# Optimization experiments

Measured on AMD Instinct MI355X. Metric: run time of the kernel, lower is better.

The kernel has to match this reference:

```python
import jax, jax.numpy as jnp
import numpy as np

B, T, A, P = 128, 128, 16, 4
D, H, Q, QI, V = 256, 512, 128, 512, 64
NUM_TRICKS = 13
SIGNAL_PHASE = 1
# static phase routing: contiguous blocks of T/P positions per phase (phase_mask buffer)
PHASE_ID = (np.arange(T) * P // T).astype(np.int32)
_DECAY = 0.6
_nt_left = NUM_TRICKS - np.arange(NUM_TRICKS, dtype=np.float32)
P_SIGNAL = ((1.0 - _DECAY) / (1.0 - _DECAY ** _nt_left)).astype(np.float32)


def setup_inputs() -> dict:
    key = jax.random.key(0)
    ks = jax.random.split(key, 12)
    a = jax.random.randint(ks[0], (B, T, A, 3), 0, V, dtype=jnp.int32)
    pad = (jax.random.uniform(ks[1], (B, T, A)) < 0.3) & (jnp.arange(A) >= 1)
    valid_actions = jnp.where(pad[..., None], -1, a)
    phase = jnp.broadcast_to(jnp.asarray(PHASE_ID), (B, T)).astype(jnp.int32)
    trick = jax.random.randint(ks[2], (B, T), 0, NUM_TRICKS, dtype=jnp.int32)
    backbone_embed = jax.random.normal(ks[3], (B, T, QI), jnp.float32)
    s = lambda k, shape, fan: jax.random.normal(k, shape, jnp.float32) / np.float32(np.sqrt(fan))
    return dict(
        backbone_embed=backbone_embed, valid_actions=valid_actions, phase=phase, trick=trick,
        emb0=s(ks[4], (V, D), D), emb1=s(ks[5], (V, D), D), emb2=s(ks[6], (V, D), D),
        ln_g=jnp.ones((D,), jnp.float32), ln_b=jnp.zeros((D,), jnp.float32),
        kW1=s(ks[7], (P, D, H), D), kb1=jnp.zeros((P, H), jnp.float32),
        kW2=s(ks[8], (P, H, H), H), kb2=jnp.zeros((P, H), jnp.float32),
        kW3=s(ks[9], (P, H, Q), H), kb3=jnp.zeros((P, Q), jnp.float32),
        qW=s(ks[10], (P, QI, Q), QI), qb=jnp.zeros((P, Q), jnp.float32),
    )


def _forward(backbone_embed, valid_actions, phase, trick,
             emb0, emb1, emb2, ln_g, ln_b,
             kW1, kb1, kW2, kb2, kW3, kb3, qW, qb):
    pid = PHASE_ID  # static (T,) routing -> gather per-position phase params (same math as mask gather/scatter)
    idx = jnp.clip(valid_actions, 0, V - 1)
    x = emb0[idx[..., 0]] + emb1[idx[..., 1]] + emb2[idx[..., 2]]  # (B,T,A,D) action embed
    mu = jnp.mean(x, -1, keepdims=True)
    var = jnp.var(x, -1, keepdims=True)
    x = (x - mu) * jax.lax.rsqrt(var + 1e-5) * ln_g + ln_b  # key LayerNorm
    # phase-branched key MLP (BranchedFF over MLP)
    h = jax.nn.relu(jnp.einsum('btad,tdh->btah', x, kW1[pid]) + kb1[pid][None, :, None, :])
    h = jax.nn.relu(jnp.einsum('btah,thg->btag', h, kW2[pid]) + kb2[pid][None, :, None, :])
    keyv = jnp.einsum('btah,thq->btaq', h, kW3[pid]) + kb3[pid][None, :, None, :]  # (B,T,A,Q)
    # phase-branched query Linear (BranchedFF over Linear)
    query = jnp.einsum('btd,tdq->btq', backbone_embed, qW[pid]) + qb[pid][None]  # (B,T,Q)
    attn = jnp.einsum('btq,btaq->bta', query, keyv) / np.float32(np.sqrt(Q))
    invalid = valid_actions[..., 0] == -1
    attn = jnp.where(invalid, -jnp.inf, attn)
    # no-signal log-weight
    n_valid = jnp.sum(~invalid, -1).astype(attn.dtype)  # (B,T)
    p_s = jnp.asarray(P_SIGNAL)[trick]
    wgt = jnp.log(jnp.maximum((1.0 - p_s) / p_s * (n_valid - 1.0), 1e-5))
    wgt = jnp.where(n_valid == 1.0, 0.0, wgt)
    attn = attn.at[..., 0].add(jnp.where(phase == SIGNAL_PHASE, wgt, 0.0))
    return jax.nn.log_softmax(attn, axis=-1)


def reference(backbone_embed, valid_actions, phase, trick,
              emb0, emb1, emb2, ln_g, ln_b,
              kW1, kb1, kW2, kb2, kW3, kb3, qW, qb):
    return _forward(backbone_embed, valid_actions, phase, trick,
                    emb0, emb1, emb2, ln_g, ln_b,
                    kW1, kb1, kW2, kb2, kW3, kb3, qW, qb)
```

## Files before the change

### kernel.cpp

```cpp
#include <hip/hip_runtime.h>
#include <hip/hip_bf16.h>
#include <cmath>

constexpr int Bc = 128, Tc = 128, Ac = 16;
constexpr int Dc = 256, Hc = 512, Qc = 128, QIc = 512, Vc = 64, NTk = 13;
constexpr float NEG_BIG = -1e30f;
constexpr float ACT_SCALE = 16.f;
constexpr float ACC_SCALE = 1.f / 256.f;
constexpr float ACC_TO_ACT = 1.f / 16.f;

typedef unsigned int uint;
typedef uint uint2v __attribute__((ext_vector_type(2)));
typedef int i32x8 __attribute__((ext_vector_type(8)));
typedef float f32x4 __attribute__((ext_vector_type(4)));
typedef float f32x16 __attribute__((ext_vector_type(16)));

#define MFMA128(a, b, c) __builtin_amdgcn_mfma_scale_f32_16x16x128_f8f6f4( \
    (a), (b), (c), 0, 0, 0, 0x7F7F7F7F, 0, 0x7F7F7F7F)
#define MFMA32(a, b, c) __builtin_amdgcn_mfma_scale_f32_32x32x64_f8f6f4( \
    (a), (b), (c), 0, 0, 0, 0x7F7F7F7F, 0, 0x7F7F7F7F)

__device__ __forceinline__ unsigned short f2bfu(float f) {
  __hip_bfloat16 h = __float2bfloat16(f);
  return *(unsigned short*)&h;
}
__device__ __forceinline__ float bf2f(short s) {
  return __uint_as_float(((unsigned)(unsigned short)s) << 16);
}
__device__ __forceinline__ uint pack4_fp8(float a, float b, float c, float d) {
  uint v = 0;
  v = __builtin_amdgcn_cvt_pk_fp8_f32(a, b, v, 0);
  v = __builtin_amdgcn_cvt_pk_fp8_f32(c, d, v, 1);
  return v;
}

__global__ void transform_all(const float* __restrict__ kW1, const float* __restrict__ kW2,
                              const float* __restrict__ kW3, const float* __restrict__ qW,
                              int* __restrict__ kW1f, int* __restrict__ kW2f,
                              int* __restrict__ kW3f, int* __restrict__ qWf) {
  int id = blockIdx.x * 256 + threadIdx.x;
  int jh = id >> 16;
  int gid = id & 65535;
  const float* W;
  int* dst;
  int NT, KC, N, local;
  bool big;
  if (gid < 16384) {
    W = kW1; dst = kW1f; NT = 16; KC = 4; N = 512; local = gid; big = true;
  } else if (gid < 49152) {
    W = kW2; dst = kW2f; NT = 16; KC = 8; N = 512; local = gid - 16384; big = true;
  } else if (gid < 57344) {
    W = kW3; dst = kW3f; NT = 4; KC = 8; N = 128; local = gid - 49152; big = true;
  } else {
    W = qW; dst = qWf; NT = 8; KC = 4; N = 128; local = gid - 57344; big = false;
  }
  int lane = local & 63;
  int frag = local >> 6;
  int kc = frag % KC;
  int rest = frag / KC;
  int nt = rest % NT;
  int pp = rest / NT;
  int K = KC * (big ? 64 : 128);
  int n, k0;
  if (big) { n = nt * 32 + (lane & 31); k0 = kc * 64 + (lane >> 5) * 32; }
  else     { n = nt * 16 + (lane & 15); k0 = kc * 128 + (lane >> 4) * 32; }
  k0 += jh * 16;
  const float* src = W + ((size_t)pp * K + k0) * N + n;
  int4 v;
  int vv[4];
#pragma unroll
  for (int jj = 0; jj < 4; ++jj) {
    float f0 = src[(size_t)(4 * jj + 0) * N] * ACT_SCALE;
    float f1 = src[(size_t)(4 * jj + 1) * N] * ACT_SCALE;
    float f2 = src[(size_t)(4 * jj + 2) * N] * ACT_SCALE;
    float f3 = src[(size_t)(4 * jj + 3) * N] * ACT_SCALE;
    vv[jj] = (int)pack4_fp8(f0, f1, f2, f3);
  }
  v.x = vv[0]; v.y = vv[1]; v.z = vv[2]; v.w = vv[3];
  *(int4*)(dst + (size_t)local * 8 + jh * 4) = v;
}

template <int KC, int AT, bool RELU, int OUTMODE, int SIN, int SOUT>
__device__ __forceinline__ void layer32r(
    const char* __restrict__ aB, void* __restrict__ o0,
    const int* __restrict__ Wfi, const float* __restrict__ bias,
    int nt0, int at0, int lane) {
  const int row = lane & 31, q = lane >> 5;
  const char* apA = aB + row * SIN + q * 32 + at0 * 32 * SIN;
  const int* wp = Wfi + (size_t)nt0 * KC * 512 + lane * 8;

  f32x16 acc[AT];
#pragma unroll
  for (int at = 0; at < AT; ++at)
#pragma unroll
    for (int r = 0; r < 16; ++r) acc[at][r] = 0.f;

#pragma unroll 1
  for (int kc = 0; kc < KC; ++kc) {
    i32x8 wv = *(const i32x8*)(wp + kc * 512);
#pragma unroll
    for (int at = 0; at < AT; ++at) {
      const char* pa = apA + at * 32 * SIN + kc * 64;
      uint4 u0 = *(const uint4*)(pa);
      uint4 u1 = *(const uint4*)(pa + 16);
      i32x8 bf;
      bf[0] = (int)u0.x; bf[1] = (int)u0.y; bf[2] = (int)u0.z; bf[3] = (int)u0.w;
      bf[4] = (int)u1.x; bf[5] = (int)u1.y; bf[6] = (int)u1.z; bf[7] = (int)u1.w;
      acc[at] = MFMA32(wv, bf, acc[at]);
    }
  }

#pragma unroll
  for (int at = 0; at < AT; ++at) {
    const int rowout = (at0 + at) * 32 + row;
    const int tb = nt0 * 32 + 4 * q;
#pragma unroll
    for (int j = 0; j < 4; ++j) {
      const int nb = tb + 8 * j;
      float4 bv = *(const float4*)(bias + nb);
      if (OUTMODE == 0) {
        float s0 = fmaf(acc[at][4 * j + 0], ACC_TO_ACT, bv.x * ACT_SCALE);
        float s1 = fmaf(acc[at][4 * j + 1], ACC_TO_ACT, bv.y * ACT_SCALE);
        float s2 = fmaf(acc[at][4 * j + 2], ACC_TO_ACT, bv.z * ACT_SCALE);
        float s3 = fmaf(acc[at][4 * j + 3], ACC_TO_ACT, bv.w * ACT_SCALE);
        if (RELU) {
          s0 = fmaxf(s0, 0.f); s1 = fmaxf(s1, 0.f);
          s2 = fmaxf(s2, 0.f); s3 = fmaxf(s3, 0.f);
        }
        *(uint*)((char*)o0 + rowout * SOUT + nb) = pack4_fp8(s0, s1, s2, s3);
      } else {
        float s0 = fmaf(acc[at][4 * j + 0], ACC_SCALE, bv.x);
        float s1 = fmaf(acc[at][4 * j + 1], ACC_SCALE, bv.y);
        float s2 = fmaf(acc[at][4 * j + 2], ACC_SCALE, bv.z);
        float s3 = fmaf(acc[at][4 * j + 3], ACC_SCALE, bv.w);
        uint2v u;
        u.x = ((uint)f2bfu(s1) << 16) | f2bfu(s0);
        u.y = ((uint)f2bfu(s3) << 16) | f2bfu(s2);
        *(uint2v*)((short*)o0 + rowout * SOUT + nb) = u;
      }
    }
  }
}

template <int KC, int SIN, int SOUT, int CMASK>
__device__ __forceinline__ void layer128r(
    const char* __restrict__ aB, float* __restrict__ o0,
    const int* __restrict__ Wfi, const float* __restrict__ bias,
    int nt0, int lane) {
  const int c = lane & 15, q = lane >> 4;
  const int sw = (c & 1) << 4;
  const char* ap = aB + (c & CMASK) * SIN + q * 32;
  const int* wp = Wfi + (size_t)nt0 * KC * 512 + lane * 8;

  f32x4 acc;
#pragma unroll
  for (int r = 0; r < 4; ++r) acc[r] = 0.f;

#pragma unroll 1
  for (int kc = 0; kc < KC; ++kc) {
    i32x8 wv = *(const i32x8*)(wp + kc * 512);
    const char* pa = ap + kc * 128;
    uint4 u0 = *(const uint4*)(pa + sw);
    uint4 u1 = *(const uint4*)(pa + (16 ^ sw));
    i32x8 bf;
    bf[0] = (int)u0.x; bf[1] = (int)u0.y; bf[2] = (int)u0.z; bf[3] = (int)u0.w;
    bf[4] = (int)u1.x; bf[5] = (int)u1.y; bf[6] = (int)u1.z; bf[7] = (int)u1.w;
    acc = MFMA128(wv, bf, acc);
  }

  const int nb = nt0 * 16 + 4 * q;
  float4 bv = *(const float4*)(bias + nb);
  if (c < 4) {
    float4 st;
    st.x = fmaf(acc[0], ACC_SCALE, bv.x);
    st.y = fmaf(acc[1], ACC_SCALE, bv.y);
    st.z = fmaf(acc[2], ACC_SCALE, bv.z);
    st.w = fmaf(acc[3], ACC_SCALE, bv.w);
    *(float4*)(o0 + c * SOUT + nb) = st;
  }
}

constexpr int SX = 272;
constexpr int SH = 528;
constexpr int SBE = 544;
constexpr int SKV = 136;
constexpr int SQY = 132;

__global__ __launch_bounds__(1024, 8) void policy_main(
    const float* __restrict__ be, const int* __restrict__ va,
    const int* __restrict__ phase, const int* __restrict__ trick,
    const float* __restrict__ emb0, const float* __restrict__ emb1,
    const float* __restrict__ emb2, const float* __restrict__ ln_g,
    const float* __restrict__ ln_b,
    const float* __restrict__ kb1, const float* __restrict__ kb2,
    const float* __restrict__ kb3, const float* __restrict__ qb,
    const int* __restrict__ kW1f, const int* __restrict__ kW2f,
    const int* __restrict__ kW3f, const int* __restrict__ qWf,
    float* __restrict__ out) {
  __shared__ __align__(16) char bufA[64 * SH];
  __shared__ __align__(16) char bufB[64 * SH];
  __shared__ __align__(16) char beAb[4 * SBE];
  __shared__ __align__(16) float QYs[4 * SQY];
  __shared__ float attn_s[64];
  __shared__ int inval_s[64];
  __shared__ int ph_s[4], tr_s[4];

  char* Xs = bufA;
  char* H2 = bufA;
  char* H1 = bufB;
  short* KV = (short*)bufB;

  const int tid = threadIdx.x;
  const int lane = tid & 63;
  const int wu = __builtin_amdgcn_readfirstlane(tid >> 6);
  const int p = blockIdx.x & 3;
  const int g = blockIdx.x >> 2;
  const int b = g >> 3;
  const int t0 = p * 32 + (g & 7) * 4;
  const int bt0 = b * Tc + t0;

  if (tid < 64) {
    inval_s[tid] = (va[((size_t)bt0 * Ac + tid) * 3] == -1);
  } else if (tid < 68) {
    ph_s[tid - 64] = phase[bt0 + tid - 64];
  } else if (tid < 72) {
    tr_s[tid - 68] = trick[bt0 + tid - 68];
  }
  if (tid < 128) {
    const int tok = tid >> 5, li = tid & 31;
    const float4* bp4 = (const float4*)(be + ((size_t)(bt0 + tok)) * QIc + li * 16);
    float4 a0 = bp4[0], a1 = bp4[1], a2 = bp4[2], a3 = bp4[3];
    uint4 v;
    v.x = pack4_fp8(a0.x * ACT_SCALE, a0.y * ACT_SCALE, a0.z * ACT_SCALE, a0.w * ACT_SCALE);
    v.y = pack4_fp8(a1.x * ACT_SCALE, a1.y * ACT_SCALE, a1.z * ACT_SCALE, a1.w * ACT_SCALE);
    v.z = pack4_fp8(a2.x * ACT_SCALE, a2.y * ACT_SCALE, a2.z * ACT_SCALE, a2.w * ACT_SCALE);
    v.w = pack4_fp8(a3.x * ACT_SCALE, a3.y * ACT_SCALE, a3.z * ACT_SCALE, a3.w * ACT_SCALE);
    *(uint4*)(beAb + tok * SBE + ((li * 16) ^ ((tok & 1) << 4))) = v;
  }
  {
    const int r = tid >> 4, part = tid & 15, d0 = part * 16;
    const int* vp = va + ((size_t)bt0 * Ac + r) * 3;
    int i0 = min(max(vp[0], 0), Vc - 1);
    int i1 = min(max(vp[1], 0), Vc - 1);
    int i2 = min(max(vp[2], 0), Vc - 1);
    const float4* e0 = (const float4*)(emb0 + i0 * Dc + d0);
    const float4* e1 = (const float4*)(emb1 + i1 * Dc + d0);
    const float4* e2 = (const float4*)(emb2 + i2 * Dc + d0);
    float xv[16];
    float sum = 0.f, ss = 0.f;
#pragma unroll
    for (int j = 0; j < 4; ++j) {
      float4 v0 = e0[j], v1 = e1[j], v2 = e2[j];
      float4 v;
      v.x = v0.x + v1.x + v2.x; v.y = v0.y + v1.y + v2.y;
      v.z = v0.z + v1.z + v2.z; v.w = v0.w + v1.w + v2.w;
      xv[j * 4 + 0] = v.x; xv[j * 4 + 1] = v.y; xv[j * 4 + 2] = v.z; xv[j * 4 + 3] = v.w;
      sum += v.x + v.y + v.z + v.w;
      ss += v.x * v.x + v.y * v.y + v.z * v.z + v.w * v.w;
    }
    sum += __shfl_xor(sum, 1); sum += __shfl_xor(sum, 2);
    sum += __shfl_xor(sum, 4); sum += __shfl_xor(sum, 8);
    ss += __shfl_xor(ss, 1);   ss += __shfl_xor(ss, 2);
    ss += __shfl_xor(ss, 4);   ss += __shfl_xor(ss, 8);
    const float mu = sum / (float)Dc;
    const float rstd = rsqrtf(ss / (float)Dc - mu * mu + 1e-5f);
    uint dw[4];
#pragma unroll
    for (int j = 0; j < 4; ++j) {
      float4 gg = *(const float4*)(ln_g + d0 + 4 * j);
      float4 bb = *(const float4*)(ln_b + d0 + 4 * j);
      float y0 = ((xv[4 * j + 0] - mu) * rstd * gg.x + bb.x) * ACT_SCALE;
      float y1 = ((xv[4 * j + 1] - mu) * rstd * gg.y + bb.y) * ACT_SCALE;
      float y2 = ((xv[4 * j + 2] - mu) * rstd * gg.z + bb.z) * ACT_SCALE;
      float y3 = ((xv[4 * j + 3] - mu) * rstd * gg.w + bb.w) * ACT_SCALE;
      dw[j] = pack4_fp8(y0, y1, y2, y3);
    }
    uint4 v;
    v.x = dw[0]; v.y = dw[1]; v.z = dw[2]; v.w = dw[3];
    *(uint4*)(Xs + r * SX + d0) = v;
  }
  __syncthreads();

  layer32r<4, 2, true, 0, SX, SH>(Xs, H1, kW1f + (size_t)p * 32768,
                                  kb1 + p * Hc, wu, 0, lane);
  __syncthreads();

  layer32r<8, 2, true, 0, SH, SH>(H1, H2, kW2f + (size_t)p * 65536,
                                  kb2 + p * Hc, wu, 0, lane);
  __syncthreads();

  if (wu < 8) {
    layer32r<8, 1, false, 1, SH, SKV>(H2, (void*)KV, kW3f + (size_t)p * 16384,
                                      kb3 + p * Qc, wu >> 1, wu & 1, lane);
  } else {
    layer128r<4, SBE, SQY, 3>(beAb, QYs, qWf + (size_t)p * 16384,
                              qb + p * Qc, wu - 8, lane);
  }
  __syncthreads();

  {
    const int r = tid >> 4, part = tid & 15, tok = r >> 4;
    uint4 kk = *(const uint4*)(KV + r * SKV + part * 8);
    const float4* qp4 = (const float4*)(QYs + tok * SQY + part * 8);
    float4 q0 = qp4[0], q1 = qp4[1];
    float s = 0.f;
    s += bf2f((short)(kk.x & 0xffff)) * q0.x;
    s += bf2f((short)(kk.x >> 16)) * q0.y;
    s += bf2f((short)(kk.y & 0xffff)) * q0.z;
    s += bf2f((short)(kk.y >> 16)) * q0.w;
    s += bf2f((short)(kk.z & 0xffff)) * q1.x;
    s += bf2f((short)(kk.z >> 16)) * q1.y;
    s += bf2f((short)(kk.w & 0xffff)) * q1.z;
    s += bf2f((short)(kk.w >> 16)) * q1.w;
    s += __shfl_xor(s, 1); s += __shfl_xor(s, 2);
    s += __shfl_xor(s, 4); s += __shfl_xor(s, 8);
    if (part == 0) attn_s[r] = s * 0.08838834764831845f;
  }
  __syncthreads();

  if (tid < 4) {
    const int tok = tid;
    const int bt = bt0 + tok;
    float av[Ac];
    int nv = 0;
#pragma unroll
    for (int a = 0; a < Ac; ++a) {
      int iv = inval_s[tok * Ac + a];
      nv += iv ? 0 : 1;
      av[a] = iv ? NEG_BIG : attn_s[tok * Ac + a];
    }
    if (ph_s[tok] == 1) {
      const int nt = NTk - tr_s[tok];
      float dp = 1.f;
      for (int i = 0; i < nt; ++i) dp *= 0.6f;
      const float ps = 0.4f / (1.f - dp);
      float wgt = (nv == 1) ? 0.f : logf(fmaxf((1.f - ps) / ps * ((float)nv - 1.f), 1e-5f));
      av[0] += wgt;
    }
    float m = NEG_BIG;
#pragma unroll
    for (int a = 0; a < Ac; ++a) m = fmaxf(m, av[a]);
    float s = 0.f;
#pragma unroll
    for (int a = 0; a < Ac; ++a) s += expf(av[a] - m);
    const float lse = logf(s) + m;
#pragma unroll
    for (int a = 0; a < Ac; ++a)
      out[bt * Ac + a] = inval_s[tok * Ac + a] ? NEG_BIG : (av[a] - lse);
  }
}

extern "C" void kernel_launch(void* const* d_in, const int* in_sizes, int n_in,
                              void* d_out, int out_size, void* d_ws, size_t ws_size,
                              hipStream_t stream) {
  const float* be   = (const float*)d_in[0];
  const int*   va   = (const int*)d_in[1];
  const int*   ph   = (const int*)d_in[2];
  const int*   tr   = (const int*)d_in[3];
  const float* emb0 = (const float*)d_in[4];
  const float* emb1 = (const float*)d_in[5];
  const float* emb2 = (const float*)d_in[6];
  const float* lng  = (const float*)d_in[7];
  const float* lnb  = (const float*)d_in[8];
  const float* kW1  = (const float*)d_in[9];
  const float* kb1  = (const float*)d_in[10];
  const float* kW2  = (const float*)d_in[11];
  const float* kb2  = (const float*)d_in[12];
  const float* kW3  = (const float*)d_in[13];
  const float* kb3  = (const float*)d_in[14];
  const float* qW   = (const float*)d_in[15];
  const float* qb   = (const float*)d_in[16];
  float* out = (float*)d_out;

  int* kW1f = (int*)d_ws;
  int* kW2f = kW1f + 131072;
  int* kW3f = kW2f + 262144;
  int* qWf  = kW3f + 65536;

  transform_all<<<512, 256, 0, stream>>>(kW1, kW2, kW3, qW, kW1f, kW2f, kW3f, qWf);

  policy_main<<<4096, 1024, 0, stream>>>(be, va, ph, tr, emb0, emb1, emb2, lng, lnb,
                                         kb1, kb2, kb3, qb, kW1f, kW2f, kW3f, qWf, out);
}
```

Measured before the change: 292.3 us.

## Swizzle LDS activations, fold scales into MFMA exponents, parallelize log-softmax

The hidden activation buffers H1/H2 are now written and read through an XOR swizzle on 16-byte chunks, meant to reduce LDS bank conflicts in the MFMA operand loads. The fixed output rescaling is folded into the MFMA scale exponents, so the epilogues drop a multiply, and bias loads are hoisted out of the per-tile loop. The final log-softmax now runs on 64 lanes with shuffle reductions instead of 4 serial threads. The swizzle has to match exactly between writer and reader layers, and the exponent encoding has to reproduce the old scaling.

```diff
diff --git a/kernel.cpp b/kernel.cpp
--- a/kernel.cpp
+++ b/kernel.cpp
@@ -6,8 +6,6 @@
 constexpr int Dc = 256, Hc = 512, Qc = 128, QIc = 512, Vc = 64, NTk = 13;
 constexpr float NEG_BIG = -1e30f;
 constexpr float ACT_SCALE = 16.f;
-constexpr float ACC_SCALE = 1.f / 256.f;
-constexpr float ACC_TO_ACT = 1.f / 16.f;
 
 typedef unsigned int uint;
 typedef uint uint2v __attribute__((ext_vector_type(2)));
@@ -15,10 +13,10 @@
 typedef float f32x4 __attribute__((ext_vector_type(4)));
 typedef float f32x16 __attribute__((ext_vector_type(16)));
 
-#define MFMA128(a, b, c) __builtin_amdgcn_mfma_scale_f32_16x16x128_f8f6f4( \
-    (a), (b), (c), 0, 0, 0, 0x7F7F7F7F, 0, 0x7F7F7F7F)
-#define MFMA32(a, b, c) __builtin_amdgcn_mfma_scale_f32_32x32x64_f8f6f4( \
-    (a), (b), (c), 0, 0, 0, 0x7F7F7F7F, 0, 0x7F7F7F7F)
+#define MFMA32S(a, b, c, SA) __builtin_amdgcn_mfma_scale_f32_32x32x64_f8f6f4( \
+    (a), (b), (c), 0, 0, 0, (int)(SA), 0, 0x7F7F7F7F)
+#define MFMA128Q(a, b, c) __builtin_amdgcn_mfma_scale_f32_16x16x128_f8f6f4( \
+    (a), (b), (c), 0, 0, 0, 0x77777777, 0, 0x7F7F7F7F)
 
 __device__ __forceinline__ unsigned short f2bfu(float f) {
   __hip_bfloat16 h = __float2bfloat16(f);
@@ -80,13 +78,15 @@
   *(int4*)(dst + (size_t)local * 8 + jh * 4) = v;
 }
 
-template <int KC, int AT, bool RELU, int OUTMODE, int SIN, int SOUT>
+template <int KC, int AT, bool RELU, int OUTMODE, int SIN, int SOUT,
+          bool SWZI, bool SWZO, unsigned SA>
 __device__ __forceinline__ void layer32r(
     const char* __restrict__ aB, void* __restrict__ o0,
     const int* __restrict__ Wfi, const float* __restrict__ bias,
     int nt0, int at0, int lane) {
   const int row = lane & 31, q = lane >> 5;
-  const char* apA = aB + row * SIN + q * 32 + at0 * 32 * SIN;
+  const unsigned swzi = SWZI ? (((unsigned)(row >> 3) & 3u) << 4) : 0u;
+  const char* apA = aB + row * SIN + at0 * 32 * SIN;
   const int* wp = Wfi + (size_t)nt0 * KC * 512 + lane * 8;
 
   f32x16 acc[AT];
@@ -100,39 +100,44 @@
     i32x8 wv = *(const i32x8*)(wp + kc * 512);
 #pragma unroll
     for (int at = 0; at < AT; ++at) {
-      const char* pa = apA + at * 32 * SIN + kc * 64;
-      uint4 u0 = *(const uint4*)(pa);
-      uint4 u1 = *(const uint4*)(pa + 16);
+      const char* pr = apA + at * 32 * SIN;
+      const unsigned X = (unsigned)(q * 32 + kc * 64);
+      uint4 u0 = *(const uint4*)(pr + (X ^ swzi));
+      uint4 u1 = *(const uint4*)(pr + ((X + 16u) ^ swzi));
       i32x8 bf;
       bf[0] = (int)u0.x; bf[1] = (int)u0.y; bf[2] = (int)u0.z; bf[3] = (int)u0.w;
       bf[4] = (int)u1.x; bf[5] = (int)u1.y; bf[6] = (int)u1.z; bf[7] = (int)u1.w;
-      acc[at] = MFMA32(wv, bf, acc[at]);
-    }
-  }
+      acc[at] = MFMA32S(wv, bf, acc[at], SA);
+    }
+  }
+
+  const int tb = nt0 * 32 + 4 * q;
+  float4 bvj[4];
+#pragma unroll
+  for (int j = 0; j < 4; ++j) bvj[j] = *(const float4*)(bias + tb + 8 * j);
 
 #pragma unroll
   for (int at = 0; at < AT; ++at) {
     const int rowout = (at0 + at) * 32 + row;
-    const int tb = nt0 * 32 + 4 * q;
+    const unsigned swzo = SWZO ? (((unsigned)(rowout >> 3) & 3u) << 4) : 0u;
 #pragma unroll
     for (int j = 0; j < 4; ++j) {
-      const int nb = tb + 8 * j;
-      float4 bv = *(const float4*)(bias + nb);
+      const unsigned nb = (unsigned)(tb + 8 * j);
       if (OUTMODE == 0) {
-        float s0 = fmaf(acc[at][4 * j + 0], ACC_TO_ACT, bv.x * ACT_SCALE);
-        float s1 = fmaf(acc[at][4 * j + 1], ACC_TO_ACT, bv.y * ACT_SCALE);
-        float s2 = fmaf(acc[at][4 * j + 2], ACC_TO_ACT, bv.z * ACT_SCALE);
-        float s3 = fmaf(acc[at][4 * j + 3], ACC_TO_ACT, bv.w * ACT_SCALE);
+        float s0 = fmaf(bvj[j].x, 16.f, acc[at][4 * j + 0]);
+        float s1 = fmaf(bvj[j].y, 16.f, acc[at][4 * j + 1]);
+        float s2 = fmaf(bvj[j].z, 16.f, acc[at][4 * j + 2]);
+        float s3 = fmaf(bvj[j].w, 16.f, acc[at][4 * j + 3]);
         if (RELU) {
           s0 = fmaxf(s0, 0.f); s1 = fmaxf(s1, 0.f);
           s2 = fmaxf(s2, 0.f); s3 = fmaxf(s3, 0.f);
         }
-        *(uint*)((char*)o0 + rowout * SOUT + nb) = pack4_fp8(s0, s1, s2, s3);
+        *(uint*)((char*)o0 + rowout * SOUT + (nb ^ swzo)) = pack4_fp8(s0, s1, s2, s3);
       } else {
-        float s0 = fmaf(acc[at][4 * j + 0], ACC_SCALE, bv.x);
-        float s1 = fmaf(acc[at][4 * j + 1], ACC_SCALE, bv.y);
-        float s2 = fmaf(acc[at][4 * j + 2], ACC_SCALE, bv.z);
-        float s3 = fmaf(acc[at][4 * j + 3], ACC_SCALE, bv.w);
+        float s0 = acc[at][4 * j + 0] + bvj[j].x;
+        float s1 = acc[at][4 * j + 1] + bvj[j].y;
+        float s2 = acc[at][4 * j + 2] + bvj[j].z;
+        float s3 = acc[at][4 * j + 3] + bvj[j].w;
         uint2v u;
         u.x = ((uint)f2bfu(s1) << 16) | f2bfu(s0);
         u.y = ((uint)f2bfu(s3) << 16) | f2bfu(s2);
@@ -165,17 +170,17 @@
     i32x8 bf;
     bf[0] = (int)u0.x; bf[1] = (int)u0.y; bf[2] = (int)u0.z; bf[3] = (int)u0.w;
     bf[4] = (int)u1.x; bf[5] = (int)u1.y; bf[6] = (int)u1.z; bf[7] = (int)u1.w;
-    acc = MFMA128(wv, bf, acc);
+    acc = MFMA128Q(wv, bf, acc);
   }
 
   const int nb = nt0 * 16 + 4 * q;
   float4 bv = *(const float4*)(bias + nb);
   if (c < 4) {
     float4 st;
-    st.x = fmaf(acc[0], ACC_SCALE, bv.x);
-    st.y = fmaf(acc[1], ACC_SCALE, bv.y);
-    st.z = fmaf(acc[2], ACC_SCALE, bv.z);
-    st.w = fmaf(acc[3], ACC_SCALE, bv.w);
+    st.x = acc[0] + bv.x;
+    st.y = acc[1] + bv.y;
+    st.z = acc[2] + bv.z;
+    st.w = acc[3] + bv.w;
     *(float4*)(o0 + c * SOUT + nb) = st;
   }
 }
@@ -281,17 +286,17 @@
   }
   __syncthreads();
 
-  layer32r<4, 2, true, 0, SX, SH>(Xs, H1, kW1f + (size_t)p * 32768,
-                                  kb1 + p * Hc, wu, 0, lane);
-  __syncthreads();
-
-  layer32r<8, 2, true, 0, SH, SH>(H1, H2, kW2f + (size_t)p * 65536,
-                                  kb2 + p * Hc, wu, 0, lane);
+  layer32r<4, 2, true, 0, SX, SH, false, true, 0x7B7B7B7Bu>(
+      Xs, H1, kW1f + (size_t)p * 32768, kb1 + p * Hc, wu, 0, lane);
+  __syncthreads();
+
+  layer32r<8, 2, true, 0, SH, SH, true, true, 0x7B7B7B7Bu>(
+      H1, H2, kW2f + (size_t)p * 65536, kb2 + p * Hc, wu, 0, lane);
   __syncthreads();
 
   if (wu < 8) {
-    layer32r<8, 1, false, 1, SH, SKV>(H2, (void*)KV, kW3f + (size_t)p * 16384,
-                                      kb3 + p * Qc, wu >> 1, wu & 1, lane);
+    layer32r<8, 1, false, 1, SH, SKV, true, false, 0x77777777u>(
+        H2, (void*)KV, kW3f + (size_t)p * 16384, kb3 + p * Qc, wu >> 1, wu & 1, lane);
   } else {
     layer128r<4, SBE, SQY, 3>(beAb, QYs, qWf + (size_t)p * 16384,
                               qb + p * Qc, wu - 8, lane);
@@ -318,35 +323,32 @@
   }
   __syncthreads();
 
-  if (tid < 4) {
-    const int tok = tid;
+  if (tid < 64) {
+    const int tok = tid >> 4, a = tid & 15;
     const int bt = bt0 + tok;
-    float av[Ac];
-    int nv = 0;
-#pragma unroll
-    for (int a = 0; a < Ac; ++a) {
-      int iv = inval_s[tok * Ac + a];
-      nv += iv ? 0 : 1;
-      av[a] = iv ? NEG_BIG : attn_s[tok * Ac + a];
-    }
-    if (ph_s[tok] == 1) {
+    const int iv = inval_s[tid];
+    float av = iv ? NEG_BIG : attn_s[tid];
+    int inv = iv;
+    inv += __shfl_xor(inv, 1); inv += __shfl_xor(inv, 2);
+    inv += __shfl_xor(inv, 4); inv += __shfl_xor(inv, 8);
+    const int nv = 16 - inv;
+    if (a == 0 && ph_s[tok] == 1) {
       const int nt = NTk - tr_s[tok];
       float dp = 1.f;
       for (int i = 0; i < nt; ++i) dp *= 0.6f;
       const float ps = 0.4f / (1.f - dp);
       float wgt = (nv == 1) ? 0.f : logf(fmaxf((1.f - ps) / ps * ((float)nv - 1.f), 1e-5f));
-      av[0] += wgt;
-    }
-    float m = NEG_BIG;
-#pragma unroll
-    for (int a = 0; a < Ac; ++a) m = fmaxf(m, av[a]);
-    float s = 0.f;
-#pragma unroll
-    for (int a = 0; a < Ac; ++a) s += expf(av[a] - m);
-    const float lse = logf(s) + m;
-#pragma unroll
-    for (int a = 0; a < Ac; ++a)
-      out[bt * Ac + a] = inval_s[tok * Ac + a] ? NEG_BIG : (av[a] - lse);
+      av += wgt;
+    }
+    float m = av;
+    m = fmaxf(m, __shfl_xor(m, 1)); m = fmaxf(m, __shfl_xor(m, 2));
+    m = fmaxf(m, __shfl_xor(m, 4)); m = fmaxf(m, __shfl_xor(m, 8));
+    float e = expf(av - m);
+    float se = e;
+    se += __shfl_xor(se, 1); se += __shfl_xor(se, 2);
+    se += __shfl_xor(se, 4); se += __shfl_xor(se, 8);
+    const float lse = logf(se) + m;
+    out[bt * Ac + a] = iv ? NEG_BIG : (av - lse);
   }
 }
 
```

New measurement: 298.7 us. 1.02x slower.
